# Optimization experiments

Measured on AMD Instinct MI355X. Metric: run time of the kernel, lower is better.

## Reference

```python
import jax, jax.numpy as jnp
import numpy as np
from jax import lax

NEG = -1e9  # stand-in for -inf that keeps gradients finite
T, V, L = 2048, 32000, 8


def setup_inputs() -> dict:
    key = jax.random.key(0)
    k1, k2, k3 = jax.random.split(key, 3)
    # log piece probabilities (valid distribution in log space)
    log_piece_probs = jax.nn.log_softmax(jax.random.normal(k1, (V,), dtype=jnp.float32))
    # match_idx[t, j] = vocab index of the (unique) piece matching sequence[t:t+j+1], or -1
    match_idx = jax.random.randint(k2, (T, L), 0, V, dtype=jnp.int32)
    keep = jax.random.uniform(k3, (T, L)) < 0.3
    keep = keep.at[:, 0].set(True)  # length-1 (single char) pieces always match -> segmentable
    in_range = (jnp.arange(T)[:, None] + jnp.arange(1, L + 1)[None, :]) <= T
    match_idx = jnp.where(keep & in_range, match_idx, -1)
    return {"log_piece_probs": log_piece_probs, "match_idx": match_idx}


def _forward(log_piece_probs, match_idx):
    T_, L_ = match_idx.shape
    V_ = log_piece_probs.shape[0]
    valid = match_idx >= 0
    # w[t, j] = log p(piece matching at pos t with length j+1), NEG if no match
    w = jnp.where(valid, log_piece_probs[jnp.clip(match_idx, 0)], NEG)  # [T, L]
    # wrev[r, j] = w[r - j, j]: contribution ending at position n = r+1 from length j+1
    wrev = jnp.stack(
        [jnp.pad(w[:, j], (j, 0), constant_values=NEG)[:T_] for j in range(L_)], axis=1
    )  # [T, L]

    # forward pass: alpha[n] = logsumexp_l alpha[n-l] + w[n-l, l-1], rolling buffer of last L alphas
    def astep(buf, wr):
        a = jax.nn.logsumexp(buf[::-1] + wr)  # buf[::-1][j] = alpha[n-1-j]
        return jnp.concatenate([buf[1:], a[None]]), a

    abuf0 = jnp.concatenate([jnp.full((L_ - 1,), NEG, jnp.float32), jnp.zeros((1,), jnp.float32)])
    _, a_rest = lax.scan(astep, abuf0, wrev)
    alpha = jnp.concatenate([jnp.zeros((1,), jnp.float32), a_rest])  # [T+1], alpha[0]=0

    # backward pass: beta[t] = logsumexp_l w[t, l-1] + beta[t+l], rolling buffer of next L betas
    def bstep(buf, wt):
        b = jax.nn.logsumexp(wt + buf)  # buf[j] = beta[t+1+j]
        return jnp.concatenate([b[None], buf[:-1]]), b

    bbuf0 = jnp.concatenate([jnp.zeros((1,), jnp.float32), jnp.full((L_ - 1,), NEG, jnp.float32)])
    _, b_rest = lax.scan(bstep, bbuf0, w, reverse=True)
    beta = jnp.concatenate([b_rest, jnp.zeros((1,), jnp.float32)])  # [T+1], beta[T]=0

    # posterior: P[t, i] = exp(alpha[t] + log p_i + beta[t+len] - alpha[T])
    nxt = jnp.arange(T_)[:, None] + jnp.arange(1, L_ + 1)[None, :]  # [T, L]
    beta_next = beta[jnp.clip(nxt, 0, T_)]
    logP = alpha[:T_, None] + w + beta_next - alpha[T_]
    vals = jnp.where(valid, jnp.exp(logP), 0.0)  # [T, L]
    P = jnp.zeros((T_, V_), jnp.float32).at[
        jnp.arange(T_)[:, None], jnp.clip(match_idx, 0)
    ].add(vals)
    return P


def reference(log_piece_probs, match_idx):
    return _forward(log_piece_probs, match_idx)
```

## Files before the change

### kernel.cpp

```cpp
#include <hip/hip_runtime.h>


#define NEGV -1e9f
#define LOG2E 1.4426950408889634f
constexpr int T = 2048;
constexpr int L = 8;
constexpr int V = 32000;
constexpr int NCH = 64;
constexpr int K = 32;
constexpr int BLK = 512;
constexpr int FILLB = 4096;
constexpr int N4 = T * V / 4;
constexpr int CH4 = N4 / FILLB;

typedef float vfloat4 __attribute__((ext_vector_type(4)));

__device__ __forceinline__ float hexp2(float x) { return __builtin_amdgcn_exp2f(x); }
__device__ __forceinline__ float hlog2(float x) { return __builtin_amdgcn_logf(x); }

__device__ __forceinline__ float lse8v(float t0, float t1, float t2, float t3,
                                       float t4, float t5, float t6, float t7) {
    float m = fmaxf(fmaxf(fmaxf(t0, t1), fmaxf(t2, t3)),
                    fmaxf(fmaxf(t4, t5), fmaxf(t6, t7)));
    float s = hexp2(t0 - m) + hexp2(t1 - m) + hexp2(t2 - m) + hexp2(t3 - m)
            + hexp2(t4 - m) + hexp2(t5 - m) + hexp2(t6 - m) + hexp2(t7 - m);
    return m + hlog2(s);
}

__global__ __launch_bounds__(BLK) void scan_fill_kernel(
        const float* __restrict__ logp, const int* __restrict__ midx,
        float* __restrict__ out, float* __restrict__ alpha, float* __restrict__ beta,
        float* __restrict__ wf, float* __restrict__ wb) {
    const int tid = threadIdx.x;
    const int bx = blockIdx.x;

    if (bx >= 2) {
        vfloat4 z = (vfloat4)0.f;
        vfloat4* o4 = (vfloat4*)out;
        const int base4 = (bx - 2) * CH4;
        const int end4 = base4 + CH4;
        for (int i = base4 + tid; i < end4; i += BLK)
            __builtin_nontemporal_store(z, &o4[i]);
        return;
    }

    __shared__ __align__(16) float sPm[NCH * 64];
    __shared__ float sVst[(NCH + 1) * 8];

    float* w = (bx == 0) ? wf : wb;
    if (bx == 0) {
        for (int o = tid; o < T * L; o += BLK) {
            int r = o >> 3, j = o & 7, t = r - j;
            float v = NEGV;
            if (t >= 0) { int m = midx[(t << 3) + j]; if (m >= 0) v = logp[m] * LOG2E; }
            wf[o] = v;
        }
        if (tid == 0) alpha[0] = 0.f;
    } else {
        for (int o = tid; o < T * L; o += BLK) {
            int s = o >> 3, j = o & 7, t = T - 1 - s;
            int m = midx[(t << 3) + j];
            wb[o] = (m >= 0) ? logp[m] * LOG2E : NEGV;
        }
        if (tid == 0) beta[T] = 0.f;
    }
    __syncthreads();

    {
        const int c = tid >> 3, col = tid & 7;
        float q[8];
#pragma unroll
        for (int i = 0; i < 8; ++i) q[i] = (i == col) ? 0.f : NEGV;
        const float4* wr4 = (const float4*)(w + c * K * 8);
        float4 c0 = wr4[0], c1 = wr4[1];
        float4 b0 = wr4[2], b1 = wr4[3];
        for (int k = 0; k < K; ++k) {
            float4 a0, a1;
            if (k + 2 < K) { a0 = wr4[(k + 2) * 2]; a1 = wr4[(k + 2) * 2 + 1]; }
            float top = lse8v(c0.x + q[0], c0.y + q[1], c0.z + q[2], c0.w + q[3],
                              c1.x + q[4], c1.y + q[5], c1.z + q[6], c1.w + q[7]);
#pragma unroll
            for (int i = 7; i > 0; --i) q[i] = q[i - 1];
            q[0] = top;
            c0 = b0; c1 = b1; b0 = a0; b1 = a1;
        }
#pragma unroll
        for (int i = 0; i < 8; ++i) sPm[c * 64 + i * 8 + col] = q[i];
    }
    __syncthreads();

    if (tid < 8) {
        const int r = tid;
        float v = (r == 0) ? 0.f : NEGV;
        for (int cc = 0; cc < NCH; ++cc) {
            sVst[cc * 8 + r] = v;
            float4 r0 = *(const float4*)&sPm[cc * 64 + r * 8];
            float4 r1 = *(const float4*)&sPm[cc * 64 + r * 8 + 4];
            float vb0 = __shfl(v, 0, 8), vb1 = __shfl(v, 1, 8);
            float vb2 = __shfl(v, 2, 8), vb3 = __shfl(v, 3, 8);
            float vb4 = __shfl(v, 4, 8), vb5 = __shfl(v, 5, 8);
            float vb6 = __shfl(v, 6, 8), vb7 = __shfl(v, 7, 8);
            v = lse8v(r0.x + vb0, r0.y + vb1, r0.z + vb2, r0.w + vb3,
                      r1.x + vb4, r1.y + vb5, r1.z + vb6, r1.w + vb7);
        }
        sVst[NCH * 8 + r] = v;
    }
    __syncthreads();

    if (tid < NCH) {
        const int cc = tid;
        float ab[8];
#pragma unroll
        for (int i = 0; i < 8; ++i) ab[i] = sVst[cc * 8 + i];
        const float4* wr4 = (const float4*)(w + cc * K * 8);
        float4 c0 = wr4[0], c1 = wr4[1];
        float4 b0 = wr4[2], b1 = wr4[3];
        for (int k = 0; k < K; ++k) {
            float4 a0, a1;
            if (k + 2 < K) { a0 = wr4[(k + 2) * 2]; a1 = wr4[(k + 2) * 2 + 1]; }
            float val = lse8v(c0.x + ab[0], c0.y + ab[1], c0.z + ab[2], c0.w + ab[3],
                              c1.x + ab[4], c1.y + ab[5], c1.z + ab[6], c1.w + ab[7]);
            int s = cc * K + k;
            if (bx == 0) alpha[s + 1] = val;
            else         beta[T - 1 - s] = val;
#pragma unroll
            for (int i = 7; i > 0; --i) ab[i] = ab[i - 1];
            ab[0] = val;
            c0 = b0; c1 = b1; b0 = a0; b1 = a1;
        }
    }
}

__global__ __launch_bounds__(256) void scatter_kernel(
        const float* __restrict__ logp, const int* __restrict__ midx,
        float* __restrict__ out, const float* __restrict__ alpha,
        const float* __restrict__ beta) {
    int i = blockIdx.x * blockDim.x + threadIdx.x;
    if (i >= T * L) return;
    int m = midx[i];
    if (m < 0) return;
    int t = i >> 3, j = i & 7;
    int nx = t + j + 1;
    if (nx > T) nx = T;
    float lp2 = alpha[t] + logp[m] * LOG2E + beta[nx] - alpha[T];
    atomicAdd(&out[(size_t)t * V + m], hexp2(lp2));
}

extern "C" void kernel_launch(void* const* d_in, const int* in_sizes, int n_in,
                              void* d_out, int out_size, void* d_ws, size_t ws_size,
                              hipStream_t stream) {
    const float* logp = (const float*)d_in[0];
    const int*   midx = (const int*)d_in[1];
    float* out = (float*)d_out;

    float* ws    = (float*)d_ws;
    float* alpha = ws;
    float* beta  = alpha + 2064;
    float* wf    = beta + 2064;
    float* wb    = wf + 16384;

    scan_fill_kernel<<<dim3(2 + FILLB), BLK, 0, stream>>>(logp, midx, out, alpha, beta, wf, wb);
    scatter_kernel<<<dim3((T * L) / 256), 256, 0, stream>>>(logp, midx, out, alpha, beta);
}
```

Measured before the change: 310.9 us.

## Halve block size, compute two transfer columns per thread, vectorize weight build, prefetch sPm

Block size drops from 512 to 256. Each chunk thread in the parallel scan phase now carries two columns of the 8x8 transfer matrix, so 4 threads cover a chunk instead of 8. The weight-array construction writes float4 vectors. The serial combine loop prefetches the next chunk's matrix rows from shared memory before doing the shuffles. The aim is to cut the per-block cost of the latency-bound scan blocks and of the zero-fill blocks, at the price of more work per thread and fewer threads per fill block.

```diff
diff --git a/kernel.cpp b/kernel.cpp
--- a/kernel.cpp
+++ b/kernel.cpp
@@ -8,7 +8,7 @@
 constexpr int V = 32000;
 constexpr int NCH = 64;
 constexpr int K = 32;
-constexpr int BLK = 512;
+constexpr int BLK = 256;
 constexpr int FILLB = 4096;
 constexpr int N4 = T * V / 4;
 constexpr int CH4 = N4 / FILLB;
@@ -49,59 +49,84 @@
 
     float* w = (bx == 0) ? wf : wb;
     if (bx == 0) {
-        for (int o = tid; o < T * L; o += BLK) {
-            int r = o >> 3, j = o & 7, t = r - j;
-            float v = NEGV;
-            if (t >= 0) { int m = midx[(t << 3) + j]; if (m >= 0) v = logp[m] * LOG2E; }
-            wf[o] = v;
+        for (int oo = tid; oo < T * 2; oo += BLK) {
+            int r = oo >> 1, j0 = (oo & 1) * 4;
+            vfloat4 v;
+#pragma unroll
+            for (int u = 0; u < 4; ++u) {
+                int j = j0 + u, t = r - j;
+                float x = NEGV;
+                if (t >= 0) { int m = midx[(t << 3) + j]; if (m >= 0) x = logp[m] * LOG2E; }
+                v[u] = x;
+            }
+            ((vfloat4*)wf)[oo] = v;
         }
         if (tid == 0) alpha[0] = 0.f;
     } else {
-        for (int o = tid; o < T * L; o += BLK) {
-            int s = o >> 3, j = o & 7, t = T - 1 - s;
-            int m = midx[(t << 3) + j];
-            wb[o] = (m >= 0) ? logp[m] * LOG2E : NEGV;
+        for (int oo = tid; oo < T * 2; oo += BLK) {
+            int s = oo >> 1, j0 = (oo & 1) * 4, t = T - 1 - s;
+            vfloat4 v;
+#pragma unroll
+            for (int u = 0; u < 4; ++u) {
+                int m = midx[(t << 3) + j0 + u];
+                v[u] = (m >= 0) ? logp[m] * LOG2E : NEGV;
+            }
+            ((vfloat4*)wb)[oo] = v;
         }
         if (tid == 0) beta[T] = 0.f;
     }
     __syncthreads();
 
     {
-        const int c = tid >> 3, col = tid & 7;
-        float q[8];
+        const int c = tid >> 2, sub = tid & 3;
+        float q0[8], q1[8];
 #pragma unroll
-        for (int i = 0; i < 8; ++i) q[i] = (i == col) ? 0.f : NEGV;
+        for (int i = 0; i < 8; ++i) {
+            q0[i] = (i == sub) ? 0.f : NEGV;
+            q1[i] = (i == sub + 4) ? 0.f : NEGV;
+        }
         const float4* wr4 = (const float4*)(w + c * K * 8);
         float4 c0 = wr4[0], c1 = wr4[1];
         float4 b0 = wr4[2], b1 = wr4[3];
         for (int k = 0; k < K; ++k) {
             float4 a0, a1;
             if (k + 2 < K) { a0 = wr4[(k + 2) * 2]; a1 = wr4[(k + 2) * 2 + 1]; }
-            float top = lse8v(c0.x + q[0], c0.y + q[1], c0.z + q[2], c0.w + q[3],
-                              c1.x + q[4], c1.y + q[5], c1.z + q[6], c1.w + q[7]);
+            float top0 = lse8v(c0.x + q0[0], c0.y + q0[1], c0.z + q0[2], c0.w + q0[3],
+                               c1.x + q0[4], c1.y + q0[5], c1.z + q0[6], c1.w + q0[7]);
+            float top1 = lse8v(c0.x + q1[0], c0.y + q1[1], c0.z + q1[2], c0.w + q1[3],
+                               c1.x + q1[4], c1.y + q1[5], c1.z + q1[6], c1.w + q1[7]);
 #pragma unroll
-            for (int i = 7; i > 0; --i) q[i] = q[i - 1];
-            q[0] = top;
+            for (int i = 7; i > 0; --i) { q0[i] = q0[i - 1]; q1[i] = q1[i - 1]; }
+            q0[0] = top0; q1[0] = top1;
             c0 = b0; c1 = b1; b0 = a0; b1 = a1;
         }
 #pragma unroll
-        for (int i = 0; i < 8; ++i) sPm[c * 64 + i * 8 + col] = q[i];
+        for (int i = 0; i < 8; ++i) {
+            sPm[c * 64 + i * 8 + sub] = q0[i];
+            sPm[c * 64 + i * 8 + sub + 4] = q1[i];
+        }
     }
     __syncthreads();
 
     if (tid < 8) {
         const int r = tid;
         float v = (r == 0) ? 0.f : NEGV;
+        float4 r0 = *(const float4*)&sPm[r * 8];
+        float4 r1 = *(const float4*)&sPm[r * 8 + 4];
         for (int cc = 0; cc < NCH; ++cc) {
             sVst[cc * 8 + r] = v;
-            float4 r0 = *(const float4*)&sPm[cc * 64 + r * 8];
-            float4 r1 = *(const float4*)&sPm[cc * 64 + r * 8 + 4];
+            float4 n0, n1;
+            if (cc + 1 < NCH) {
+                n0 = *(const float4*)&sPm[(cc + 1) * 64 + r * 8];
+                n1 = *(const float4*)&sPm[(cc + 1) * 64 + r * 8 + 4];
+            }
             float vb0 = __shfl(v, 0, 8), vb1 = __shfl(v, 1, 8);
             float vb2 = __shfl(v, 2, 8), vb3 = __shfl(v, 3, 8);
             float vb4 = __shfl(v, 4, 8), vb5 = __shfl(v, 5, 8);
             float vb6 = __shfl(v, 6, 8), vb7 = __shfl(v, 7, 8);
             v = lse8v(r0.x + vb0, r0.y + vb1, r0.z + vb2, r0.w + vb3,
                       r1.x + vb4, r1.y + vb5, r1.z + vb6, r1.w + vb7);
+            r0 = n0; r1 = n1;
         }
         sVst[NCH * 8 + r] = v;
     }
```

After: 323.8 us. 1.04x slower.

## Stage scan weights and outputs in shared memory instead of global workspace

Applied to the files above, without the earlier changes.

Moves the per-direction weight table from global workspace into padded LDS, and buffers the alpha/beta results in LDS so they are written out coalesced at the end. It also prefetches the next chunk's matrix in the serial combine step, and swaps the nontemporal zero-fill stores for plain float4 stores. The aim is to shorten the latency-bound scan blocks, which sit on the critical path. The cost is extra LDS use per block, which also applies to the fill blocks and may reduce their occupancy. Dropping the nontemporal hint may change cache behaviour for the 262MB fill.

```diff
diff --git a/kernel.cpp b/kernel.cpp
--- a/kernel.cpp
+++ b/kernel.cpp
@@ -12,8 +12,7 @@
 constexpr int FILLB = 4096;
 constexpr int N4 = T * V / 4;
 constexpr int CH4 = N4 / FILLB;
-
-typedef float vfloat4 __attribute__((ext_vector_type(4)));
+constexpr int CPAD = K * 8 + 4;
 
 __device__ __forceinline__ float hexp2(float x) { return __builtin_amdgcn_exp2f(x); }
 __device__ __forceinline__ float hlog2(float x) { return __builtin_amdgcn_logf(x); }
@@ -29,40 +28,37 @@
 
 __global__ __launch_bounds__(BLK) void scan_fill_kernel(
         const float* __restrict__ logp, const int* __restrict__ midx,
-        float* __restrict__ out, float* __restrict__ alpha, float* __restrict__ beta,
-        float* __restrict__ wf, float* __restrict__ wb) {
+        float* __restrict__ out, float* __restrict__ alpha, float* __restrict__ beta) {
     const int tid = threadIdx.x;
     const int bx = blockIdx.x;
 
     if (bx >= 2) {
-        vfloat4 z = (vfloat4)0.f;
-        vfloat4* o4 = (vfloat4*)out;
+        float4 z = make_float4(0.f, 0.f, 0.f, 0.f);
+        float4* o4 = (float4*)out;
         const int base4 = (bx - 2) * CH4;
         const int end4 = base4 + CH4;
-        for (int i = base4 + tid; i < end4; i += BLK)
-            __builtin_nontemporal_store(z, &o4[i]);
+        for (int i = base4 + tid; i < end4; i += BLK) o4[i] = z;
         return;
     }
 
+    __shared__ __align__(16) float sW[NCH * CPAD];
     __shared__ __align__(16) float sPm[NCH * 64];
     __shared__ float sVst[(NCH + 1) * 8];
+    __shared__ float sOut[NCH * 33];
 
-    float* w = (bx == 0) ? wf : wb;
     if (bx == 0) {
         for (int o = tid; o < T * L; o += BLK) {
             int r = o >> 3, j = o & 7, t = r - j;
             float v = NEGV;
             if (t >= 0) { int m = midx[(t << 3) + j]; if (m >= 0) v = logp[m] * LOG2E; }
-            wf[o] = v;
+            sW[(r >> 5) * CPAD + (r & 31) * 8 + j] = v;
         }
-        if (tid == 0) alpha[0] = 0.f;
     } else {
         for (int o = tid; o < T * L; o += BLK) {
             int s = o >> 3, j = o & 7, t = T - 1 - s;
             int m = midx[(t << 3) + j];
-            wb[o] = (m >= 0) ? logp[m] * LOG2E : NEGV;
+            sW[(s >> 5) * CPAD + (s & 31) * 8 + j] = (m >= 0) ? logp[m] * LOG2E : NEGV;
         }
-        if (tid == 0) beta[T] = 0.f;
     }
     __syncthreads();
 
@@ -71,12 +67,15 @@
         float q[8];
 #pragma unroll
         for (int i = 0; i < 8; ++i) q[i] = (i == col) ? 0.f : NEGV;
-        const float4* wr4 = (const float4*)(w + c * K * 8);
-        float4 c0 = wr4[0], c1 = wr4[1];
-        float4 b0 = wr4[2], b1 = wr4[3];
+        const float* wc = &sW[c * CPAD];
+        float4 c0 = *(const float4*)(wc + 0), c1 = *(const float4*)(wc + 4);
+        float4 b0 = *(const float4*)(wc + 8), b1 = *(const float4*)(wc + 12);
         for (int k = 0; k < K; ++k) {
             float4 a0, a1;
-            if (k + 2 < K) { a0 = wr4[(k + 2) * 2]; a1 = wr4[(k + 2) * 2 + 1]; }
+            if (k + 2 < K) {
+                a0 = *(const float4*)(wc + (k + 2) * 8);
+                a1 = *(const float4*)(wc + (k + 2) * 8 + 4);
+            }
             float top = lse8v(c0.x + q[0], c0.y + q[1], c0.z + q[2], c0.w + q[3],
                               c1.x + q[4], c1.y + q[5], c1.z + q[6], c1.w + q[7]);
 #pragma unroll
@@ -92,16 +91,22 @@
     if (tid < 8) {
         const int r = tid;
         float v = (r == 0) ? 0.f : NEGV;
+        float4 r0 = *(const float4*)&sPm[r * 8];
+        float4 r1 = *(const float4*)&sPm[r * 8 + 4];
         for (int cc = 0; cc < NCH; ++cc) {
             sVst[cc * 8 + r] = v;
-            float4 r0 = *(const float4*)&sPm[cc * 64 + r * 8];
-            float4 r1 = *(const float4*)&sPm[cc * 64 + r * 8 + 4];
+            float4 n0, n1;
+            if (cc + 1 < NCH) {
+                n0 = *(const float4*)&sPm[(cc + 1) * 64 + r * 8];
+                n1 = *(const float4*)&sPm[(cc + 1) * 64 + r * 8 + 4];
+            }
             float vb0 = __shfl(v, 0, 8), vb1 = __shfl(v, 1, 8);
             float vb2 = __shfl(v, 2, 8), vb3 = __shfl(v, 3, 8);
             float vb4 = __shfl(v, 4, 8), vb5 = __shfl(v, 5, 8);
             float vb6 = __shfl(v, 6, 8), vb7 = __shfl(v, 7, 8);
             v = lse8v(r0.x + vb0, r0.y + vb1, r0.z + vb2, r0.w + vb3,
                       r1.x + vb4, r1.y + vb5, r1.z + vb6, r1.w + vb7);
+            r0 = n0; r1 = n1;
         }
         sVst[NCH * 8 + r] = v;
     }
@@ -112,22 +117,36 @@
         float ab[8];
 #pragma unroll
         for (int i = 0; i < 8; ++i) ab[i] = sVst[cc * 8 + i];
-        const float4* wr4 = (const float4*)(w + cc * K * 8);
-        float4 c0 = wr4[0], c1 = wr4[1];
-        float4 b0 = wr4[2], b1 = wr4[3];
+        const float* wc = &sW[cc * CPAD];
+        float4 c0 = *(const float4*)(wc + 0), c1 = *(const float4*)(wc + 4);
+        float4 b0 = *(const float4*)(wc + 8), b1 = *(const float4*)(wc + 12);
         for (int k = 0; k < K; ++k) {
             float4 a0, a1;
-            if (k + 2 < K) { a0 = wr4[(k + 2) * 2]; a1 = wr4[(k + 2) * 2 + 1]; }
+            if (k + 2 < K) {
+                a0 = *(const float4*)(wc + (k + 2) * 8);
+                a1 = *(const float4*)(wc + (k + 2) * 8 + 4);
+            }
             float val = lse8v(c0.x + ab[0], c0.y + ab[1], c0.z + ab[2], c0.w + ab[3],
                               c1.x + ab[4], c1.y + ab[5], c1.z + ab[6], c1.w + ab[7]);
-            int s = cc * K + k;
-            if (bx == 0) alpha[s + 1] = val;
-            else         beta[T - 1 - s] = val;
+            sOut[cc * 33 + k] = val;
 #pragma unroll
             for (int i = 7; i > 0; --i) ab[i] = ab[i - 1];
             ab[0] = val;
             c0 = b0; c1 = b1; b0 = a0; b1 = a1;
         }
+    }
+    __syncthreads();
+
+    if (bx == 0) {
+        for (int o = tid; o < T; o += BLK)
+            alpha[o + 1] = sOut[(o >> 5) * 33 + (o & 31)];
+        if (tid == 0) alpha[0] = 0.f;
+    } else {
+        for (int o = tid; o < T; o += BLK) {
+            int s = T - 1 - o;
+            beta[o] = sOut[(s >> 5) * 33 + (s & 31)];
+        }
+        if (tid == 0) beta[T] = 0.f;
     }
 }
 
@@ -156,9 +175,7 @@
     float* ws    = (float*)d_ws;
     float* alpha = ws;
     float* beta  = alpha + 2064;
-    float* wf    = beta + 2064;
-    float* wb    = wf + 16384;
 
-    scan_fill_kernel<<<dim3(2 + FILLB), BLK, 0, stream>>>(logp, midx, out, alpha, beta, wf, wb);
+    scan_fill_kernel<<<dim3(2 + FILLB), BLK, 0, stream>>>(logp, midx, out, alpha, beta);
     scatter_kernel<<<dim3((T * L) / 256), 256, 0, stream>>>(logp, midx, out, alpha, beta);
 }
```

Result: faster. 286.2 us (-7.9%).
